# Optimization experiments

Hardware: AMD Instinct MI355X
Metric: run time of the kernel (lower is better)

## Reference

```python
import jax, jax.numpy as jnp
import numpy as np

H = 128  # hidden_dim
F = 64   # node_feat_dim


def setup_inputs() -> dict:
    key = jax.random.key(0)
    ks = jax.random.split(key, 24)
    N, E, NR, NT = 50000, 400000, 20000, 20000
    inp = {
        "mol_x": jax.random.normal(ks[0], (N, F), jnp.float32),
        "pos": jax.random.normal(ks[1], (N, 3), jnp.float32),
        "reaction_x": jax.random.normal(ks[2], (NR, F), jnp.float32),
        "target_x": jax.random.normal(ks[3], (NT, F), jnp.float32),
        "edge_index": jax.random.randint(ks[4], (2, E), 0, N, jnp.int32),
    }
    def lin(k, fan_in, fan_out):
        s = 1.0 / np.sqrt(fan_in)
        kw, kb = jax.random.split(k)
        W = jax.random.uniform(kw, (fan_in, fan_out), jnp.float32, -s, s)
        b = jax.random.uniform(kb, (fan_out,), jnp.float32, -s, s)
        return W, b
    inp["W_node"], inp["b_node"] = lin(ks[5], F, H)
    inp["W_att1"], inp["b_att1"] = lin(ks[6], 2 * H + 3, H)
    inp["W_att2"], inp["b_att2"] = lin(ks[7], H, 1)
    inp["W_upd"], inp["b_upd"] = lin(ks[8], H, H)
    inp["Wy1"], inp["by1"] = lin(ks[9], H, 64)
    inp["Wy2"], inp["by2"] = lin(ks[10], 64, 1)
    inp["Wa1"], inp["ba1"] = lin(ks[11], H, 64)
    inp["Wa2"], inp["ba2"] = lin(ks[12], 64, 1)
    return inp


def reference(mol_x, pos, reaction_x, target_x, edge_index,
              W_node, b_node, W_att1, b_att1, W_att2, b_att2,
              W_upd, b_upd, Wy1, by1, Wy2, by2, Wa1, ba1, Wa2, ba2):
    N = mol_x.shape[0]
    # node encoder
    h = mol_x @ W_node + b_node                      # [N, H]
    src, dst = edge_index[0], edge_index[1]          # PyG: x_j = source, x_i = target
    x_j = h[src]                                      # [E, H]
    x_i = h[dst]                                      # [E, H]
    dist = pos[dst] - pos[src]                        # [E, 3]
    cat = jnp.concatenate([x_i, x_j, dist], axis=1)   # [E, 2H+3]
    s = jax.nn.relu(cat @ W_att1 + b_att1) @ W_att2 + b_att2  # [E, 1]
    att = jax.nn.softmax(s, axis=0)                   # global softmax over edges (dim=0)
    msg = x_j * att                                   # [E, H]
    aggr = jax.ops.segment_sum(msg, dst, num_segments=N)  # scatter-add -> [N, H]
    mol_feats = aggr @ W_upd + b_upd                  # [N, H]
    # heads on reaction / target graphs
    rh = reaction_x @ W_node + b_node
    th = target_x @ W_node + b_node
    pred_yield = (jax.nn.relu(rh @ Wy1 + by1) @ Wy2 + by2).squeeze(-1)
    pred_activity = (jax.nn.relu(th @ Wa1 + ba1) @ Wa2 + ba2).squeeze(-1)
    return pred_yield, pred_activity, mol_feats
```

## Files before the change

### kernel.cpp

```cpp
#include <hip/hip_runtime.h>
#include <hip/hip_bf16.h>

typedef unsigned short ushort_t;
typedef __attribute__((ext_vector_type(8))) short s16x8;
typedef __attribute__((ext_vector_type(4))) float f32x4;

__device__ inline unsigned short f2bf(float x) {
    unsigned u = __float_as_uint(x);
    return (unsigned short)((u + 0x7FFFu + ((u >> 16) & 1u)) >> 16);
}
__device__ inline float bflo(unsigned u) { return __uint_as_float(u << 16); }
__device__ inline float bfhi(unsigned u) { return __uint_as_float(u & 0xffff0000u); }

__device__ inline void pack_one(const float* __restrict__ W, int K, int N,
                                ushort_t* __restrict__ dst, int g) {
    int KT = K / 32;
    int nt = g / (KT * 64);
    int rem = g % (KT * 64);
    int kt = rem / 64, lane = rem % 64;
    int n = nt * 16 + (lane & 15);
    int kbase = kt * 32 + ((lane >> 4) << 3);
    ushort_t tmp[8];
#pragma unroll
    for (int j = 0; j < 8; ++j) tmp[j] = f2bf(W[(size_t)(kbase + j) * N + n]);
    uint4 pk;
    pk.x = tmp[0] | ((unsigned)tmp[1] << 16);
    pk.y = tmp[2] | ((unsigned)tmp[3] << 16);
    pk.z = tmp[4] | ((unsigned)tmp[5] << 16);
    pk.w = tmp[6] | ((unsigned)tmp[7] << 16);
    *(uint4*)&dst[(size_t)g * 8] = pk;
}

__global__ void convert_w(const float* __restrict__ Wn, const float* __restrict__ W1,
                          const float* __restrict__ Wu, const float* __restrict__ Wy1,
                          const float* __restrict__ Wa1,
                          ushort_t* __restrict__ Wnb, ushort_t* __restrict__ W1tb,
                          ushort_t* __restrict__ W1mb, ushort_t* __restrict__ Wub,
                          ushort_t* __restrict__ Wy1b, ushort_t* __restrict__ Wa1b) {
    int t = blockIdx.x * 256 + threadIdx.x;
    if (t < 1024)       pack_one(Wn, 64, 128, Wnb, t);
    else if (t < 3072)  pack_one(W1, 128, 128, W1tb, t - 1024);
    else if (t < 5120)  pack_one(W1 + 128 * 128, 128, 128, W1mb, t - 3072);
    else if (t < 7168)  pack_one(Wu, 128, 128, Wub, t - 5120);
    else if (t < 8192)  pack_one(Wy1, 128, 64, Wy1b, t - 7168);
    else if (t < 9216)  pack_one(Wa1, 128, 64, Wa1b, t - 8192);
}

__global__ void encode_pq(const float* __restrict__ x, const ushort_t* __restrict__ Wnb,
                          const float* __restrict__ bn, const ushort_t* __restrict__ W1tb,
                          const ushort_t* __restrict__ W1mb, const float* __restrict__ b1,
                          ushort_t* __restrict__ hb, ushort_t* __restrict__ P,
                          ushort_t* __restrict__ Q, int nrows) {
    __shared__ ushort_t ldsX[16 * 72];
    __shared__ ushort_t ldsH[16 * 136];
    int t = threadIdx.x;
    int r0 = blockIdx.x * 16;
    {
        int row = t >> 4, c4 = (t & 15) * 4;
        float4 v = *(const float4*)&x[(size_t)(r0 + row) * 64 + c4];
        uint2 pk;
        pk.x = f2bf(v.x) | ((unsigned)f2bf(v.y) << 16);
        pk.y = f2bf(v.z) | ((unsigned)f2bf(v.w) << 16);
        *(uint2*)&ldsX[row * 72 + c4] = pk;
    }
    __syncthreads();
    int w = t >> 6, lane = t & 63;
    int c = lane & 15, q = lane >> 4;
    int ntA = w, ntB = w + 4;
    {
        f32x4 acc0 = {0.f, 0.f, 0.f, 0.f}, acc1 = acc0;
#pragma unroll
        for (int kt = 0; kt < 2; ++kt) {
            s16x8 a = *(const s16x8*)&ldsX[c * 72 + kt * 32 + q * 8];
            s16x8 b0 = *(const s16x8*)&Wnb[((ntA * 2 + kt) * 64 + lane) * 8];
            s16x8 b1v = *(const s16x8*)&Wnb[((ntB * 2 + kt) * 64 + lane) * 8];
            acc0 = __builtin_amdgcn_mfma_f32_16x16x32_bf16(a, b0, acc0, 0, 0, 0);
            acc1 = __builtin_amdgcn_mfma_f32_16x16x32_bf16(a, b1v, acc1, 0, 0, 0);
        }
        float bi0 = bn[ntA * 16 + c], bi1 = bn[ntB * 16 + c];
#pragma unroll
        for (int r = 0; r < 4; ++r) {
            int row = r0 + q * 4 + r;
            ushort_t h0 = f2bf(acc0[r] + bi0), h1 = f2bf(acc1[r] + bi1);
            ldsH[(q * 4 + r) * 136 + ntA * 16 + c] = h0;
            ldsH[(q * 4 + r) * 136 + ntB * 16 + c] = h1;
            if (row < nrows) {
                hb[(size_t)row * 128 + ntA * 16 + c] = h0;
                hb[(size_t)row * 128 + ntB * 16 + c] = h1;
            }
        }
    }
    __syncthreads();
    {
        f32x4 p0 = {0.f, 0.f, 0.f, 0.f}, p1 = p0, q0 = p0, q1 = p0;
#pragma unroll
        for (int kt = 0; kt < 4; ++kt) {
            s16x8 a = *(const s16x8*)&ldsH[c * 136 + kt * 32 + q * 8];
            s16x8 bp0 = *(const s16x8*)&W1tb[((ntA * 4 + kt) * 64 + lane) * 8];
            s16x8 bp1 = *(const s16x8*)&W1tb[((ntB * 4 + kt) * 64 + lane) * 8];
            s16x8 bq0 = *(const s16x8*)&W1mb[((ntA * 4 + kt) * 64 + lane) * 8];
            s16x8 bq1 = *(const s16x8*)&W1mb[((ntB * 4 + kt) * 64 + lane) * 8];
            p0 = __builtin_amdgcn_mfma_f32_16x16x32_bf16(a, bp0, p0, 0, 0, 0);
            p1 = __builtin_amdgcn_mfma_f32_16x16x32_bf16(a, bp1, p1, 0, 0, 0);
            q0 = __builtin_amdgcn_mfma_f32_16x16x32_bf16(a, bq0, q0, 0, 0, 0);
            q1 = __builtin_amdgcn_mfma_f32_16x16x32_bf16(a, bq1, q1, 0, 0, 0);
        }
        float bi0 = b1[ntA * 16 + c], bi1 = b1[ntB * 16 + c];
#pragma unroll
        for (int r = 0; r < 4; ++r) {
            int row = r0 + q * 4 + r;
            if (row < nrows) {
                P[(size_t)row * 128 + ntA * 16 + c] = f2bf(p0[r] + bi0);
                P[(size_t)row * 128 + ntB * 16 + c] = f2bf(p1[r] + bi1);
                Q[(size_t)row * 128 + ntA * 16 + c] = f2bf(q0[r]);
                Q[(size_t)row * 128 + ntB * 16 + c] = f2bf(q1[r]);
            }
        }
    }
}

__global__ void edge_score(const ushort_t* __restrict__ P, const ushort_t* __restrict__ Q,
                           const float* __restrict__ pos, const int* __restrict__ src,
                           const int* __restrict__ dst, const float* __restrict__ W1b,
                           const float* __restrict__ W2, const float* __restrict__ b2,
                           float* __restrict__ s_out, int* __restrict__ counts,
                           float* __restrict__ redm, float* __restrict__ rede, int E) {
    __shared__ float wsh[4 * 128];
    __shared__ float smm[256], sme[256];
    int t = threadIdx.x;
    for (int i = t; i < 384; i += 256) wsh[i] = W1b[i];
    if (t < 128) wsh[384 + t] = W2[t];
    __syncthreads();
    int w = t >> 6, lane = t & 63;
    int g = lane >> 4;
    int c = lane & 15;
    float w0[8], w1[8], w2[8], wv[8];
#pragma unroll
    for (int j = 0; j < 8; ++j) {
        w0[j] = wsh[c * 8 + j];
        w1[j] = wsh[128 + c * 8 + j];
        w2[j] = wsh[256 + c * 8 + j];
        wv[j] = wsh[384 + c * 8 + j];
    }
    float b2v = b2[0];
    int base = blockIdx.x * 64 + w * 16;
    float m = -1e30f, ev = 0.f;
#pragma unroll
    for (int it = 0; it < 4; ++it) {
        int e = base + it * 4 + g;
        bool valid = e < E;
        int ee = valid ? e : (E - 1);
        int sa = src[ee], da = dst[ee];
        uint4 pr = *(const uint4*)&P[(size_t)da * 128 + c * 8];
        uint4 qr = *(const uint4*)&Q[(size_t)sa * 128 + c * 8];
        float d0 = pos[da * 3]     - pos[sa * 3];
        float d1 = pos[da * 3 + 1] - pos[sa * 3 + 1];
        float d2 = pos[da * 3 + 2] - pos[sa * 3 + 2];
        unsigned pw[4] = {pr.x, pr.y, pr.z, pr.w};
        unsigned qw[4] = {qr.x, qr.y, qr.z, qr.w};
        float v = 0.f;
#pragma unroll
        for (int jj = 0; jj < 4; ++jj) {
            float pe = bflo(pw[jj]) + bflo(qw[jj])
                     + d0 * w0[2 * jj] + d1 * w1[2 * jj] + d2 * w2[2 * jj];
            float po = bfhi(pw[jj]) + bfhi(qw[jj])
                     + d0 * w0[2 * jj + 1] + d1 * w1[2 * jj + 1] + d2 * w2[2 * jj + 1];
            v += fmaxf(pe, 0.f) * wv[2 * jj] + fmaxf(po, 0.f) * wv[2 * jj + 1];
        }
#pragma unroll
        for (int off = 1; off < 16; off <<= 1) v += __shfl_xor(v, off, 64);
        float sv = v + b2v;
        if (c == 0 && valid) {
            s_out[e] = sv;
            atomicAdd(&counts[da], 1);
            float nm = fmaxf(m, sv);
            ev = ev * __expf(m - nm) + __expf(sv - nm);
            m = nm;
        }
    }
    smm[t] = m; sme[t] = ev; __syncthreads();
    for (int off = 128; off > 0; off >>= 1) {
        if (t < off) {
            float m1 = smm[t], m2 = smm[t + off];
            float e1 = sme[t], e2 = sme[t + off];
            float M = fmaxf(m1, m2);
            smm[t] = M;
            sme[t] = e1 * __expf(m1 - M) + e2 * __expf(m2 - M);
        }
        __syncthreads();
    }
    if (t == 0) { redm[blockIdx.x] = smm[0]; rede[blockIdx.x] = sme[0]; }
}

__global__ void smax2(const float* __restrict__ redm, const float* __restrict__ rede,
                      float* __restrict__ scal, int nb) {
    __shared__ float smm[256], sme[256];
    int t = threadIdx.x;
    float m = -1e30f, ev = 0.f;
    for (int i = t; i < nb; i += 256) {
        float m2 = redm[i], e2 = rede[i];
        float M = fmaxf(m, m2);
        ev = ev * __expf(m - M) + e2 * __expf(m2 - M);
        m = M;
    }
    smm[t] = m; sme[t] = ev; __syncthreads();
    for (int off = 128; off > 0; off >>= 1) {
        if (t < off) {
            float m1 = smm[t], m2 = smm[t + off];
            float e1 = sme[t], e2 = sme[t + off];
            float M = fmaxf(m1, m2);
            smm[t] = M;
            sme[t] = e1 * __expf(m1 - M) + e2 * __expf(m2 - M);
        }
        __syncthreads();
    }
    if (t == 0) { scal[0] = smm[0]; scal[1] = 1.f / sme[0]; }
}

__global__ void scan1(const int* __restrict__ counts, int* __restrict__ offs,
                      int* __restrict__ partials, int N) {
    __shared__ int sm[256];
    int i = blockIdx.x * 256 + threadIdx.x;
    int v = (i < N) ? counts[i] : 0;
    sm[threadIdx.x] = v; __syncthreads();
    for (int off = 1; off < 256; off <<= 1) {
        int add = (threadIdx.x >= off) ? sm[threadIdx.x - off] : 0;
        __syncthreads();
        sm[threadIdx.x] += add;
        __syncthreads();
    }
    if (i < N) offs[i] = sm[threadIdx.x] - v;
    if (threadIdx.x == 255) partials[blockIdx.x] = sm[255];
}

__global__ void scan2(int* __restrict__ partials, int nb) {
    __shared__ int sm[256];
    int v = (threadIdx.x < nb) ? partials[threadIdx.x] : 0;
    sm[threadIdx.x] = v; __syncthreads();
    for (int off = 1; off < 256; off <<= 1) {
        int add = (threadIdx.x >= off) ? sm[threadIdx.x - off] : 0;
        __syncthreads();
        sm[threadIdx.x] += add;
        __syncthreads();
    }
    if (threadIdx.x < nb) partials[threadIdx.x] = sm[threadIdx.x] - v;
}

__global__ void scan3(int* __restrict__ offs, int* __restrict__ cursor,
                      const int* __restrict__ partials, int N) {
    int i = blockIdx.x * 256 + threadIdx.x;
    if (i < N) {
        int v = offs[i] + partials[blockIdx.x];
        offs[i] = v;
        cursor[i] = v;
    }
}

__global__ void fill_csr(const int* __restrict__ src, const int* __restrict__ dst,
                         int* __restrict__ cursor, int2* __restrict__ csr, int E) {
    int e = blockIdx.x * 256 + threadIdx.x;
    if (e >= E) return;
    int p = atomicAdd(&cursor[dst[e]], 1);
    csr[p] = make_int2(e, src[e]);
}

__global__ void gather_upd(const ushort_t* __restrict__ hb, const int2* __restrict__ csr,
                           const int* __restrict__ offs, const int* __restrict__ deg,
                           const float* __restrict__ s, const float* __restrict__ scal,
                           const ushort_t* __restrict__ Wub, const float* __restrict__ bu,
                           float* __restrict__ C, int N) {
    __shared__ ushort_t ldsA[16 * 136];
    int t = threadIdx.x;
    int w = t >> 6, lane = t & 63;
    int half = lane >> 5, l32 = lane & 31;
    int r0 = blockIdx.x * 16;
    float m = scal[0], inv = scal[1];
#pragma unroll
    for (int i = 0; i < 4; ++i) {
        int node = r0 + w * 4 + i;
        float a0 = 0.f, a1 = 0.f, a2 = 0.f, a3 = 0.f;
        if (node < N) {
            int start = offs[node], d = deg[node];
            for (int k = half; k < d; k += 2) {
                int2 es = csr[start + k];
                float att = __expf(s[es.x] - m) * inv;
                uint2 hq = *(const uint2*)&hb[(size_t)es.y * 128 + l32 * 4];
                a0 += bflo(hq.x) * att;
                a1 += bfhi(hq.x) * att;
                a2 += bflo(hq.y) * att;
                a3 += bfhi(hq.y) * att;
            }
        }
        a0 += __shfl_xor(a0, 32, 64);
        a1 += __shfl_xor(a1, 32, 64);
        a2 += __shfl_xor(a2, 32, 64);
        a3 += __shfl_xor(a3, 32, 64);
        if (half == 0) {
            uint2 pk;
            pk.x = f2bf(a0) | ((unsigned)f2bf(a1) << 16);
            pk.y = f2bf(a2) | ((unsigned)f2bf(a3) << 16);
            *(uint2*)&ldsA[(w * 4 + i) * 136 + l32 * 4] = pk;
        }
    }
    __syncthreads();
    int c = lane & 15, q = lane >> 4;
    int ntA = w, ntB = w + 4;
    f32x4 acc0 = {0.f, 0.f, 0.f, 0.f}, acc1 = acc0;
#pragma unroll
    for (int kt = 0; kt < 4; ++kt) {
        s16x8 a = *(const s16x8*)&ldsA[c * 136 + kt * 32 + q * 8];
        s16x8 b0 = *(const s16x8*)&Wub[((ntA * 4 + kt) * 64 + lane) * 8];
        s16x8 b1 = *(const s16x8*)&Wub[((ntB * 4 + kt) * 64 + lane) * 8];
        acc0 = __builtin_amdgcn_mfma_f32_16x16x32_bf16(a, b0, acc0, 0, 0, 0);
        acc1 = __builtin_amdgcn_mfma_f32_16x16x32_bf16(a, b1, acc1, 0, 0, 0);
    }
    float bi0 = bu[ntA * 16 + c], bi1 = bu[ntB * 16 + c];
#pragma unroll
    for (int r = 0; r < 4; ++r) {
        int row = r0 + q * 4 + r;
        if (row < N) {
            C[(size_t)row * 128 + ntA * 16 + c] = acc0[r] + bi0;
            C[(size_t)row * 128 + ntB * 16 + c] = acc1[r] + bi1;
        }
    }
}

__global__ void head_mfma(const float* __restrict__ rx, const float* __restrict__ tx,
                          const ushort_t* __restrict__ Wnb, const float* __restrict__ bn,
                          const ushort_t* __restrict__ Wy1b, const float* __restrict__ by1,
                          const float* __restrict__ Wy2, const float* __restrict__ by2,
                          const ushort_t* __restrict__ Wa1b, const float* __restrict__ ba1,
                          const float* __restrict__ Wa2, const float* __restrict__ ba2,
                          float* __restrict__ out, int nb1, int NR, int NT) {
    __shared__ ushort_t ldsA[16 * 72];
    __shared__ ushort_t ldsB[16 * 136];
    __shared__ float part[64];
    int blk = blockIdx.x;
    const float* x; const ushort_t* W1b; const float* b1; const float* W2; const float* b2;
    float* o; int r0, nrows;
    if (blk < nb1) { x = rx; W1b = Wy1b; b1 = by1; W2 = Wy2; b2 = by2; o = out; r0 = blk * 16; nrows = NR; }
    else { x = tx; W1b = Wa1b; b1 = ba1; W2 = Wa2; b2 = ba2; o = out + NR; r0 = (blk - nb1) * 16; nrows = NT; }

    int t = threadIdx.x;
    {
        int row = t >> 4, c4 = (t & 15) * 4;
        float4 v = *(const float4*)&x[(size_t)(r0 + row) * 64 + c4];
        uint2 pk;
        pk.x = f2bf(v.x) | ((unsigned)f2bf(v.y) << 16);
        pk.y = f2bf(v.z) | ((unsigned)f2bf(v.w) << 16);
        *(uint2*)&ldsA[row * 72 + c4] = pk;
    }
    __syncthreads();
    int w = t >> 6, lane = t & 63;
    int c = lane & 15, q = lane >> 4;
    {
        int ntA = w, ntB = w + 4;
        f32x4 acc0 = {0.f, 0.f, 0.f, 0.f}, acc1 = acc0;
#pragma unroll
        for (int kt = 0; kt < 2; ++kt) {
            s16x8 a = *(const s16x8*)&ldsA[c * 72 + kt * 32 + q * 8];
            s16x8 b0 = *(const s16x8*)&Wnb[((ntA * 2 + kt) * 64 + lane) * 8];
            s16x8 b1v = *(const s16x8*)&Wnb[((ntB * 2 + kt) * 64 + lane) * 8];
            acc0 = __builtin_amdgcn_mfma_f32_16x16x32_bf16(a, b0, acc0, 0, 0, 0);
            acc1 = __builtin_amdgcn_mfma_f32_16x16x32_bf16(a, b1v, acc1, 0, 0, 0);
        }
        float bi0 = bn[ntA * 16 + c], bi1 = bn[ntB * 16 + c];
#pragma unroll
        for (int r = 0; r < 4; ++r) {
            int row = q * 4 + r;
            ldsB[row * 136 + ntA * 16 + c] = f2bf(acc0[r] + bi0);
            ldsB[row * 136 + ntB * 16 + c] = f2bf(acc1[r] + bi1);
        }
    }
    __syncthreads();
    {
        f32x4 acc = {0.f, 0.f, 0.f, 0.f};
#pragma unroll
        for (int kt = 0; kt < 4; ++kt) {
            s16x8 a = *(const s16x8*)&ldsB[c * 136 + kt * 32 + q * 8];
            s16x8 b0 = *(const s16x8*)&W1b[((w * 4 + kt) * 64 + lane) * 8];
            acc = __builtin_amdgcn_mfma_f32_16x16x32_bf16(a, b0, acc, 0, 0, 0);
        }
        float bi = b1[w * 16 + c], w2v = W2[w * 16 + c];
#pragma unroll
        for (int r = 0; r < 4; ++r) {
            float u = fmaxf(acc[r] + bi, 0.f) * w2v;
#pragma unroll
            for (int mm = 1; mm < 16; mm <<= 1) u += __shfl_xor(u, mm, 64);
            if (c == 0) part[w * 16 + q * 4 + r] = u;
        }
    }
    __syncthreads();
    if (t < 16) {
        int row = r0 + t;
        if (row < nrows)
            o[row] = part[t] + part[16 + t] + part[32 + t] + part[48 + t] + b2[0];
    }
}

extern "C" void kernel_launch(void* const* d_in, const int* in_sizes, int n_in,
                              void* d_out, int out_size, void* d_ws, size_t ws_size,
                              hipStream_t stream) {
    const float* mol_x      = (const float*)d_in[0];
    const float* pos        = (const float*)d_in[1];
    const float* reaction_x = (const float*)d_in[2];
    const float* target_x   = (const float*)d_in[3];
    const int*   ei         = (const int*)d_in[4];
    const float* W_node = (const float*)d_in[5];
    const float* b_node = (const float*)d_in[6];
    const float* W_att1 = (const float*)d_in[7];
    const float* b_att1 = (const float*)d_in[8];
    const float* W_att2 = (const float*)d_in[9];
    const float* b_att2 = (const float*)d_in[10];
    const float* W_upd  = (const float*)d_in[11];
    const float* b_upd  = (const float*)d_in[12];
    const float* Wy1 = (const float*)d_in[13];
    const float* by1 = (const float*)d_in[14];
    const float* Wy2 = (const float*)d_in[15];
    const float* by2 = (const float*)d_in[16];
    const float* Wa1 = (const float*)d_in[17];
    const float* ba1 = (const float*)d_in[18];
    const float* Wa2 = (const float*)d_in[19];
    const float* ba2 = (const float*)d_in[20];

    int N  = in_sizes[0] / 64;
    int E  = in_sizes[4] / 2;
    int NR = in_sizes[2] / 64;
    int NT = in_sizes[3] / 64;

    float* out = (float*)d_out;

    int nbE = (E + 63) / 64;

    char* wp = (char*)d_ws;
    ushort_t* hb = (ushort_t*)wp;  wp += (size_t)N * 128 * 2;
    ushort_t* Qb = (ushort_t*)wp;  wp += (size_t)N * 128 * 2;
    float* s     = (float*)wp;     wp += (size_t)E * 4;
    float* redm  = (float*)wp;     wp += (size_t)nbE * 4;
    float* rede  = (float*)wp;     wp += (size_t)nbE * 4;
    float* scal  = (float*)wp;     wp += 4 * 4;
    int* counts  = (int*)wp;       wp += (size_t)N * 4;
    int* offs    = (int*)wp;       wp += (size_t)N * 4;
    int* cursor  = (int*)wp;       wp += (size_t)N * 4;
    int* partials= (int*)wp;       wp += 256 * 4;
    int2* csr    = (int2*)wp;      wp += (size_t)E * 8;
    ushort_t* Wnb  = (ushort_t*)wp; wp += 8192 * 2;
    ushort_t* W1tb = (ushort_t*)wp; wp += 16384 * 2;
    ushort_t* W1mb = (ushort_t*)wp; wp += 16384 * 2;
    ushort_t* Wub  = (ushort_t*)wp; wp += 16384 * 2;
    ushort_t* Wy1b = (ushort_t*)wp; wp += 8192 * 2;
    ushort_t* Wa1b = (ushort_t*)wp; wp += 8192 * 2;
    ushort_t* Pb = (ushort_t*)(out + NR + NT);
    float* molf  = out + NR + NT;

    const int* srcp = ei;
    const int* dstp = ei + E;
    int nbN = (N + 255) / 256;

    hipMemsetAsync(counts, 0, (size_t)N * sizeof(int), stream);
    convert_w<<<36, 256, 0, stream>>>(W_node, W_att1, W_upd, Wy1, Wa1,
                                      Wnb, W1tb, W1mb, Wub, Wy1b, Wa1b);
    encode_pq<<<(N + 15) / 16, 256, 0, stream>>>(mol_x, Wnb, b_node, W1tb, W1mb, b_att1,
                                                 hb, Pb, Qb, N);
    edge_score<<<nbE, 256, 0, stream>>>(Pb, Qb, pos, srcp, dstp,
                                        W_att1 + 256 * 128, W_att2, b_att2,
                                        s, counts, redm, rede, E);
    smax2<<<1, 256, 0, stream>>>(redm, rede, scal, nbE);
    scan1<<<nbN, 256, 0, stream>>>(counts, offs, partials, N);
    scan2<<<1, 256, 0, stream>>>(partials, nbN);
    scan3<<<nbN, 256, 0, stream>>>(offs, cursor, partials, N);
    fill_csr<<<(E + 255) / 256, 256, 0, stream>>>(srcp, dstp, cursor, csr, E);
    gather_upd<<<(N + 15) / 16, 256, 0, stream>>>(hb, csr, offs, counts, s, scal,
                                                  Wub, b_upd, molf, N);
    head_mfma<<<(NR + NT) / 16, 256, 0, stream>>>(reaction_x, target_x, Wnb, b_node,
                                                  Wy1b, by1, Wy2, by2, Wa1b, ba1, Wa2, ba2,
                                                  out, NR / 16, NR, NT);
}
```

Baseline: 256.3 us.

## Build CSR before edge scoring and score edges per destination node

Moves the dst histogram into its own kernel, builds the CSR before scoring, and rewrites edge scoring to walk CSR per destination node. Each node's P row and position are then loaded once and reused across its incoming edges. Scores are stored in CSR order, so gather_upd reads them contiguously instead of indirectly via edge ids, and the CSR entry shrinks to just the source index. gather_upd also switches to 16-byte loads with four edges in flight per wave. The risk is that per-node work is imbalanced for varying degree, with one wave per node and some idle lanes, and smax2 now reduces over more blocks.

Result: slower. 279.2 us (+8.9%).

```diff
diff --git a/kernel.cpp b/kernel.cpp
--- a/kernel.cpp
+++ b/kernel.cpp
@@ -119,12 +119,65 @@
     }
 }
 
-__global__ void edge_score(const ushort_t* __restrict__ P, const ushort_t* __restrict__ Q,
-                           const float* __restrict__ pos, const int* __restrict__ src,
-                           const int* __restrict__ dst, const float* __restrict__ W1b,
-                           const float* __restrict__ W2, const float* __restrict__ b2,
-                           float* __restrict__ s_out, int* __restrict__ counts,
-                           float* __restrict__ redm, float* __restrict__ rede, int E) {
+__global__ void hist_dst(const int* __restrict__ dst, int* __restrict__ counts, int E) {
+    int e = blockIdx.x * 256 + threadIdx.x;
+    if (e < E) atomicAdd(&counts[dst[e]], 1);
+}
+
+__global__ void scan1(const int* __restrict__ counts, int* __restrict__ offs,
+                      int* __restrict__ partials, int N) {
+    __shared__ int sm[256];
+    int i = blockIdx.x * 256 + threadIdx.x;
+    int v = (i < N) ? counts[i] : 0;
+    sm[threadIdx.x] = v; __syncthreads();
+    for (int off = 1; off < 256; off <<= 1) {
+        int add = (threadIdx.x >= off) ? sm[threadIdx.x - off] : 0;
+        __syncthreads();
+        sm[threadIdx.x] += add;
+        __syncthreads();
+    }
+    if (i < N) offs[i] = sm[threadIdx.x] - v;
+    if (threadIdx.x == 255) partials[blockIdx.x] = sm[255];
+}
+
+__global__ void scan2(int* __restrict__ partials, int nb) {
+    __shared__ int sm[256];
+    int v = (threadIdx.x < nb) ? partials[threadIdx.x] : 0;
+    sm[threadIdx.x] = v; __syncthreads();
+    for (int off = 1; off < 256; off <<= 1) {
+        int add = (threadIdx.x >= off) ? sm[threadIdx.x - off] : 0;
+        __syncthreads();
+        sm[threadIdx.x] += add;
+        __syncthreads();
+    }
+    if (threadIdx.x < nb) partials[threadIdx.x] = sm[threadIdx.x] - v;
+}
+
+__global__ void scan3(int* __restrict__ offs, int* __restrict__ cursor,
+                      const int* __restrict__ partials, int N) {
+    int i = blockIdx.x * 256 + threadIdx.x;
+    if (i < N) {
+        int v = offs[i] + partials[blockIdx.x];
+        offs[i] = v;
+        cursor[i] = v;
+    }
+}
+
+__global__ void fill_csr(const int* __restrict__ src, const int* __restrict__ dst,
+                         int* __restrict__ cursor, int* __restrict__ csrc, int E) {
+    int e = blockIdx.x * 256 + threadIdx.x;
+    if (e >= E) return;
+    int p = atomicAdd(&cursor[dst[e]], 1);
+    csrc[p] = src[e];
+}
+
+__global__ void edge_score_csr(const ushort_t* __restrict__ P, const ushort_t* __restrict__ Q,
+                               const float* __restrict__ pos, const int* __restrict__ csrc,
+                               const int* __restrict__ offs, const int* __restrict__ deg,
+                               const float* __restrict__ W1b, const float* __restrict__ W2,
+                               const float* __restrict__ b2,
+                               float* __restrict__ s_csr,
+                               float* __restrict__ redm, float* __restrict__ rede, int N) {
     __shared__ float wsh[4 * 128];
     __shared__ float smm[256], sme[256];
     int t = threadIdx.x;
@@ -132,8 +185,7 @@
     if (t < 128) wsh[384 + t] = W2[t];
     __syncthreads();
     int w = t >> 6, lane = t & 63;
-    int g = lane >> 4;
-    int c = lane & 15;
+    int g = lane >> 4, c = lane & 15;
     float w0[8], w1[8], w2[8], wv[8];
 #pragma unroll
     for (int j = 0; j < 8; ++j) {
@@ -143,39 +195,40 @@
         wv[j] = wsh[384 + c * 8 + j];
     }
     float b2v = b2[0];
-    int base = blockIdx.x * 64 + w * 16;
     float m = -1e30f, ev = 0.f;
-#pragma unroll
-    for (int it = 0; it < 4; ++it) {
-        int e = base + it * 4 + g;
-        bool valid = e < E;
-        int ee = valid ? e : (E - 1);
-        int sa = src[ee], da = dst[ee];
-        uint4 pr = *(const uint4*)&P[(size_t)da * 128 + c * 8];
-        uint4 qr = *(const uint4*)&Q[(size_t)sa * 128 + c * 8];
-        float d0 = pos[da * 3]     - pos[sa * 3];
-        float d1 = pos[da * 3 + 1] - pos[sa * 3 + 1];
-        float d2 = pos[da * 3 + 2] - pos[sa * 3 + 2];
-        unsigned pw[4] = {pr.x, pr.y, pr.z, pr.w};
-        unsigned qw[4] = {qr.x, qr.y, qr.z, qr.w};
-        float v = 0.f;
-#pragma unroll
-        for (int jj = 0; jj < 4; ++jj) {
-            float pe = bflo(pw[jj]) + bflo(qw[jj])
-                     + d0 * w0[2 * jj] + d1 * w1[2 * jj] + d2 * w2[2 * jj];
-            float po = bfhi(pw[jj]) + bfhi(qw[jj])
-                     + d0 * w0[2 * jj + 1] + d1 * w1[2 * jj + 1] + d2 * w2[2 * jj + 1];
-            v += fmaxf(pe, 0.f) * wv[2 * jj] + fmaxf(po, 0.f) * wv[2 * jj + 1];
-        }
-#pragma unroll
-        for (int off = 1; off < 16; off <<= 1) v += __shfl_xor(v, off, 64);
-        float sv = v + b2v;
-        if (c == 0 && valid) {
-            s_out[e] = sv;
-            atomicAdd(&counts[da], 1);
-            float nm = fmaxf(m, sv);
-            ev = ev * __expf(m - nm) + __expf(sv - nm);
-            m = nm;
+    int node = blockIdx.x * 4 + w;
+    if (node < N) {
+        int start = offs[node], d = deg[node];
+        uint4 pr = *(const uint4*)&P[(size_t)node * 128 + c * 8];
+        float pv[8];
+        pv[0] = bflo(pr.x); pv[1] = bfhi(pr.x); pv[2] = bflo(pr.y); pv[3] = bfhi(pr.y);
+        pv[4] = bflo(pr.z); pv[5] = bfhi(pr.z); pv[6] = bflo(pr.w); pv[7] = bfhi(pr.w);
+        float pd0 = pos[node * 3], pd1 = pos[node * 3 + 1], pd2 = pos[node * 3 + 2];
+        for (int k = g; k < d; k += 4) {
+            int sa = csrc[start + k];
+            uint4 qr = *(const uint4*)&Q[(size_t)sa * 128 + c * 8];
+            float d0 = pd0 - pos[sa * 3];
+            float d1 = pd1 - pos[sa * 3 + 1];
+            float d2 = pd2 - pos[sa * 3 + 2];
+            unsigned qw[4] = {qr.x, qr.y, qr.z, qr.w};
+            float v = 0.f;
+#pragma unroll
+            for (int jj = 0; jj < 4; ++jj) {
+                float pe = pv[2 * jj] + bflo(qw[jj])
+                         + d0 * w0[2 * jj] + d1 * w1[2 * jj] + d2 * w2[2 * jj];
+                float po = pv[2 * jj + 1] + bfhi(qw[jj])
+                         + d0 * w0[2 * jj + 1] + d1 * w1[2 * jj + 1] + d2 * w2[2 * jj + 1];
+                v += fmaxf(pe, 0.f) * wv[2 * jj] + fmaxf(po, 0.f) * wv[2 * jj + 1];
+            }
+#pragma unroll
+            for (int off = 1; off < 16; off <<= 1) v += __shfl_xor(v, off, 64);
+            if (c == 0) {
+                float sv = v + b2v;
+                s_csr[start + k] = sv;
+                float nm = fmaxf(m, sv);
+                ev = ev * __expf(m - nm) + __expf(sv - nm);
+                m = nm;
+            }
         }
     }
     smm[t] = m; sme[t] = ev; __syncthreads();
@@ -217,102 +270,58 @@
     if (t == 0) { scal[0] = smm[0]; scal[1] = 1.f / sme[0]; }
 }
 
-__global__ void scan1(const int* __restrict__ counts, int* __restrict__ offs,
-                      int* __restrict__ partials, int N) {
-    __shared__ int sm[256];
-    int i = blockIdx.x * 256 + threadIdx.x;
-    int v = (i < N) ? counts[i] : 0;
-    sm[threadIdx.x] = v; __syncthreads();
-    for (int off = 1; off < 256; off <<= 1) {
-        int add = (threadIdx.x >= off) ? sm[threadIdx.x - off] : 0;
-        __syncthreads();
-        sm[threadIdx.x] += add;
-        __syncthreads();
-    }
-    if (i < N) offs[i] = sm[threadIdx.x] - v;
-    if (threadIdx.x == 255) partials[blockIdx.x] = sm[255];
-}
-
-__global__ void scan2(int* __restrict__ partials, int nb) {
-    __shared__ int sm[256];
-    int v = (threadIdx.x < nb) ? partials[threadIdx.x] : 0;
-    sm[threadIdx.x] = v; __syncthreads();
-    for (int off = 1; off < 256; off <<= 1) {
-        int add = (threadIdx.x >= off) ? sm[threadIdx.x - off] : 0;
-        __syncthreads();
-        sm[threadIdx.x] += add;
-        __syncthreads();
-    }
-    if (threadIdx.x < nb) partials[threadIdx.x] = sm[threadIdx.x] - v;
-}
-
-__global__ void scan3(int* __restrict__ offs, int* __restrict__ cursor,
-                      const int* __restrict__ partials, int N) {
-    int i = blockIdx.x * 256 + threadIdx.x;
-    if (i < N) {
-        int v = offs[i] + partials[blockIdx.x];
-        offs[i] = v;
-        cursor[i] = v;
-    }
-}
-
-__global__ void fill_csr(const int* __restrict__ src, const int* __restrict__ dst,
-                         int* __restrict__ cursor, int2* __restrict__ csr, int E) {
-    int e = blockIdx.x * 256 + threadIdx.x;
-    if (e >= E) return;
-    int p = atomicAdd(&cursor[dst[e]], 1);
-    csr[p] = make_int2(e, src[e]);
-}
-
-__global__ void gather_upd(const ushort_t* __restrict__ hb, const int2* __restrict__ csr,
+__global__ void gather_upd(const ushort_t* __restrict__ hb, const int* __restrict__ csrc,
                            const int* __restrict__ offs, const int* __restrict__ deg,
-                           const float* __restrict__ s, const float* __restrict__ scal,
+                           const float* __restrict__ s_csr, const float* __restrict__ scal,
                            const ushort_t* __restrict__ Wub, const float* __restrict__ bu,
                            float* __restrict__ C, int N) {
     __shared__ ushort_t ldsA[16 * 136];
     int t = threadIdx.x;
     int w = t >> 6, lane = t & 63;
-    int half = lane >> 5, l32 = lane & 31;
+    int g = lane >> 4, c = lane & 15;
     int r0 = blockIdx.x * 16;
     float m = scal[0], inv = scal[1];
 #pragma unroll
     for (int i = 0; i < 4; ++i) {
         int node = r0 + w * 4 + i;
-        float a0 = 0.f, a1 = 0.f, a2 = 0.f, a3 = 0.f;
+        float a[8] = {0.f, 0.f, 0.f, 0.f, 0.f, 0.f, 0.f, 0.f};
         if (node < N) {
             int start = offs[node], d = deg[node];
-            for (int k = half; k < d; k += 2) {
-                int2 es = csr[start + k];
-                float att = __expf(s[es.x] - m) * inv;
-                uint2 hq = *(const uint2*)&hb[(size_t)es.y * 128 + l32 * 4];
-                a0 += bflo(hq.x) * att;
-                a1 += bfhi(hq.x) * att;
-                a2 += bflo(hq.y) * att;
-                a3 += bfhi(hq.y) * att;
+            for (int k = g; k < d; k += 4) {
+                float att = __expf(s_csr[start + k] - m) * inv;
+                int sa = csrc[start + k];
+                uint4 hq = *(const uint4*)&hb[(size_t)sa * 128 + c * 8];
+                a[0] += bflo(hq.x) * att; a[1] += bfhi(hq.x) * att;
+                a[2] += bflo(hq.y) * att; a[3] += bfhi(hq.y) * att;
+                a[4] += bflo(hq.z) * att; a[5] += bfhi(hq.z) * att;
+                a[6] += bflo(hq.w) * att; a[7] += bfhi(hq.w) * att;
             }
         }
-        a0 += __shfl_xor(a0, 32, 64);
-        a1 += __shfl_xor(a1, 32, 64);
-        a2 += __shfl_xor(a2, 32, 64);
-        a3 += __shfl_xor(a3, 32, 64);
-        if (half == 0) {
-            uint2 pk;
-            pk.x = f2bf(a0) | ((unsigned)f2bf(a1) << 16);
-            pk.y = f2bf(a2) | ((unsigned)f2bf(a3) << 16);
-            *(uint2*)&ldsA[(w * 4 + i) * 136 + l32 * 4] = pk;
-        }
-    }
-    __syncthreads();
-    int c = lane & 15, q = lane >> 4;
+#pragma unroll
+        for (int j = 0; j < 8; ++j) {
+            a[j] += __shfl_xor(a[j], 16, 64);
+            a[j] += __shfl_xor(a[j], 32, 64);
+        }
+        if (g == 0) {
+            uint4 pk;
+            pk.x = f2bf(a[0]) | ((unsigned)f2bf(a[1]) << 16);
+            pk.y = f2bf(a[2]) | ((unsigned)f2bf(a[3]) << 16);
+            pk.z = f2bf(a[4]) | ((unsigned)f2bf(a[5]) << 16);
+            pk.w = f2bf(a[6]) | ((unsigned)f2bf(a[7]) << 16);
+            *(uint4*)&ldsA[(w * 4 + i) * 136 + c * 8] = pk;
+        }
+    }
+    __syncthreads();
+    int q = lane >> 4;
     int ntA = w, ntB = w + 4;
     f32x4 acc0 = {0.f, 0.f, 0.f, 0.f}, acc1 = acc0;
 #pragma unroll
     for (int kt = 0; kt < 4; ++kt) {
-        s16x8 a = *(const s16x8*)&ldsA[c * 136 + kt * 32 + q * 8];
+        s16x8 av = *(const s16x8*)&ldsA[c * 136 + kt * 32 + q * 8];
         s16x8 b0 = *(const s16x8*)&Wub[((ntA * 4 + kt) * 64 + lane) * 8];
         s16x8 b1 = *(const s16x8*)&Wub[((ntB * 4 + kt) * 64 + lane) * 8];
-        acc0 = __builtin_amdgcn_mfma_f32_16x16x32_bf16(a, b0, acc0, 0, 0, 0);
-        acc1 = __builtin_amdgcn_mfma_f32_16x16x32_bf16(a, b1, acc1, 0, 0, 0);
+        acc0 = __builtin_amdgcn_mfma_f32_16x16x32_bf16(av, b0, acc0, 0, 0, 0);
+        acc1 = __builtin_amdgcn_mfma_f32_16x16x32_bf16(av, b1, acc1, 0, 0, 0);
     }
     float bi0 = bu[ntA * 16 + c], bi1 = bu[ntB * 16 + c];
 #pragma unroll
@@ -430,20 +439,20 @@
 
     float* out = (float*)d_out;
 
-    int nbE = (E + 63) / 64;
+    int nbS = (N + 3) / 4;
 
     char* wp = (char*)d_ws;
     ushort_t* hb = (ushort_t*)wp;  wp += (size_t)N * 128 * 2;
     ushort_t* Qb = (ushort_t*)wp;  wp += (size_t)N * 128 * 2;
-    float* s     = (float*)wp;     wp += (size_t)E * 4;
-    float* redm  = (float*)wp;     wp += (size_t)nbE * 4;
-    float* rede  = (float*)wp;     wp += (size_t)nbE * 4;
+    float* s_csr = (float*)wp;     wp += (size_t)E * 4;
+    float* redm  = (float*)wp;     wp += (size_t)nbS * 4;
+    float* rede  = (float*)wp;     wp += (size_t)nbS * 4;
     float* scal  = (float*)wp;     wp += 4 * 4;
     int* counts  = (int*)wp;       wp += (size_t)N * 4;
     int* offs    = (int*)wp;       wp += (size_t)N * 4;
     int* cursor  = (int*)wp;       wp += (size_t)N * 4;
     int* partials= (int*)wp;       wp += 256 * 4;
-    int2* csr    = (int2*)wp;      wp += (size_t)E * 8;
+    int* csrc    = (int*)wp;       wp += (size_t)E * 4;
     ushort_t* Wnb  = (ushort_t*)wp; wp += 8192 * 2;
     ushort_t* W1tb = (ushort_t*)wp; wp += 16384 * 2;
     ushort_t* W1mb = (ushort_t*)wp; wp += 16384 * 2;
@@ -462,15 +471,16 @@
                                       Wnb, W1tb, W1mb, Wub, Wy1b, Wa1b);
     encode_pq<<<(N + 15) / 16, 256, 0, stream>>>(mol_x, Wnb, b_node, W1tb, W1mb, b_att1,
                                                  hb, Pb, Qb, N);
-    edge_score<<<nbE, 256, 0, stream>>>(Pb, Qb, pos, srcp, dstp,
-                                        W_att1 + 256 * 128, W_att2, b_att2,
-                                        s, counts, redm, rede, E);
-    smax2<<<1, 256, 0, stream>>>(redm, rede, scal, nbE);
+    hist_dst<<<(E + 255) / 256, 256, 0, stream>>>(dstp, counts, E);
     scan1<<<nbN, 256, 0, stream>>>(counts, offs, partials, N);
     scan2<<<1, 256, 0, stream>>>(partials, nbN);
     scan3<<<nbN, 256, 0, stream>>>(offs, cursor, partials, N);
-    fill_csr<<<(E + 255) / 256, 256, 0, stream>>>(srcp, dstp, cursor, csr, E);
-    gather_upd<<<(N + 15) / 16, 256, 0, stream>>>(hb, csr, offs, counts, s, scal,
+    fill_csr<<<(E + 255) / 256, 256, 0, stream>>>(srcp, dstp, cursor, csrc, E);
+    edge_score_csr<<<nbS, 256, 0, stream>>>(Pb, Qb, pos, csrc, offs, counts,
+                                            W_att1 + 256 * 128, W_att2, b_att2,
+                                            s_csr, redm, rede, N);
+    smax2<<<1, 256, 0, stream>>>(redm, rede, scal, nbS);
+    gather_upd<<<(N + 15) / 16, 256, 0, stream>>>(hb, csrc, offs, counts, s_csr, scal,
                                                   Wub, b_upd, molf, N);
     head_mfma<<<(NR + NT) / 16, 256, 0, stream>>>(reaction_x, target_x, Wnb, b_node,
                                                   Wy1b, by1, Wy2, by2, Wa1b, ba1, Wa2, ba2,
```
